# Performance work log

Measured on AMD Instinct MI355X. Metric: run time of the kernel, lower is better.

The kernel has to match this reference:

```python
import jax, jax.numpy as jnp
import numpy as np

N = 50000
E = 800000
G = 64  # number of graphs in each batch
IN_DIM = 128
HID = 64
NEG_SLOPE = 0.2


def _glorot(key, shape):
    fan = shape[0] + shape[-1] if len(shape) == 2 else int(np.prod(shape[1:])) + shape[-1]
    lim = float(np.sqrt(6.0 / fan))
    return jax.random.uniform(key, shape, jnp.float32, -lim, lim)


def setup_inputs() -> dict:
    key = jax.random.key(0)
    ks = jax.random.split(key, 16)
    x1 = jax.random.normal(ks[0], (N, IN_DIM), jnp.float32)
    x2 = jax.random.normal(ks[1], (N, IN_DIM), jnp.float32)
    edge_index1 = jax.random.randint(ks[2], (2, E), 0, N, jnp.int64)
    edge_index2 = jax.random.randint(ks[3], (2, E), 0, N, jnp.int64)
    batch1 = jnp.sort(jax.random.randint(ks[4], (N,), 0, G, jnp.int64))
    batch2 = jnp.sort(jax.random.randint(ks[5], (N,), 0, G, jnp.int64))
    # conv1: GATConv(IN_DIM, HID, heads=4)
    W1 = _glorot(ks[6], (IN_DIM, 4 * HID))
    a_src1 = _glorot(ks[7], (1, 4, HID))
    a_dst1 = _glorot(ks[8], (1, 4, HID))
    b1 = jnp.zeros((4 * HID,), jnp.float32)
    # conv2: GATConv(4*HID, HID, heads=1)
    W2 = _glorot(ks[9], (4 * HID, HID))
    a_src2 = _glorot(ks[10], (1, 1, HID))
    a_dst2 = _glorot(ks[11], (1, 1, HID))
    b2 = jnp.zeros((HID,), jnp.float32)
    return {"x1": x1, "edge_index1": edge_index1, "batch1": batch1,
            "x2": x2, "edge_index2": edge_index2, "batch2": batch2,
            "W1": W1, "a_src1": a_src1, "a_dst1": a_dst1, "b1": b1,
            "W2": W2, "a_src2": a_src2, "a_dst2": a_dst2, "b2": b2}


def gat_conv(x, src, dst, W, a_src, a_dst, b, n_nodes, heads, out_dim):
    """PyG GATConv with add_self_loops=True, negative_slope=0.2, concat=True."""
    h = (x @ W).reshape(n_nodes, heads, out_dim)            # [N,H,D]
    alpha_s = jnp.sum(h * a_src, axis=-1)                   # [N,H]
    alpha_d = jnp.sum(h * a_dst, axis=-1)                   # [N,H]
    e = alpha_s[src] + alpha_d[dst]                         # [E',H]
    e = jax.nn.leaky_relu(e, NEG_SLOPE)
    # segment softmax over incoming edges of each destination node
    e_max = jax.ops.segment_max(e, dst, num_segments=n_nodes)
    ex = jnp.exp(e - e_max[dst])
    denom = jax.ops.segment_sum(ex, dst, num_segments=n_nodes)
    alpha = ex / (denom[dst] + 1e-16)                       # [E',H]
    msg = h[src] * alpha[:, :, None]                        # [E',H,D]
    out = jax.ops.segment_sum(msg, dst, num_segments=n_nodes)
    return out.reshape(n_nodes, heads * out_dim) + b


def embed(x, edge_index, batch, W1, a_src1, a_dst1, b1, W2, a_src2, a_dst2, b2):
    loops = jnp.arange(N, dtype=edge_index.dtype)
    src = jnp.concatenate([edge_index[0], loops])
    dst = jnp.concatenate([edge_index[1], loops])
    h = jax.nn.elu(gat_conv(x, src, dst, W1, a_src1, a_dst1, b1, N, 4, HID))
    h = jax.nn.elu(gat_conv(h, src, dst, W2, a_src2, a_dst2, b2, N, 1, HID))
    # global_mean_pool over graph ids
    sums = jax.ops.segment_sum(h, batch, num_segments=G)
    cnt = jax.ops.segment_sum(jnp.ones((N,), h.dtype), batch, num_segments=G)
    return sums / jnp.maximum(cnt, 1.0)[:, None]


def reference(x1, edge_index1, batch1, x2, edge_index2, batch2,
              W1, a_src1, a_dst1, b1, W2, a_src2, a_dst2, b2):
    emb1 = embed(x1, edge_index1, batch1, W1, a_src1, a_dst1, b1, W2, a_src2, a_dst2, b2)
    emb2 = embed(x2, edge_index2, batch2, W1, a_src1, a_dst1, b1, W2, a_src2, a_dst2, b2)
    return (emb1, emb2)
```

## Files before the change

kernel.cpp:

```cpp
#include <hip/hip_runtime.h>
#include <cstdint>
#include <cstddef>

#define NNODES 50000
#define NEDGES 800000
#define NGR    64
#define INDIM  128
#define HIDD   64
#define DCAP   64
#define NBUCK  391
#define BCAP   2560

typedef __attribute__((ext_vector_type(8))) _Float16 f16x8;
typedef __attribute__((ext_vector_type(2))) _Float16 half2v;
typedef __attribute__((ext_vector_type(4))) float f32x4;
typedef __attribute__((ext_vector_type(2))) float f32x2;

__device__ __forceinline__ float lrelu(float x) { return x > 0.f ? x : 0.2f * x; }
__device__ __forceinline__ float eluf(float x)  { return x > 0.f ? x : expm1f(x); }
__device__ __forceinline__ unsigned short f2h(float x) {
    _Float16 h = (_Float16)x;
    return __builtin_bit_cast(unsigned short, h);
}
__device__ __forceinline__ float h2f(unsigned short u) {
    return (float)__builtin_bit_cast(_Float16, u);
}
__device__ __forceinline__ float h2lo(unsigned int u) {
    half2v h = __builtin_bit_cast(half2v, u);
    return (float)h.x;
}
__device__ __forceinline__ float h2hi(unsigned int u) {
    half2v h = __builtin_bit_cast(half2v, u);
    return (float)h.y;
}

__global__ void cvt_f2h(const float* __restrict__ in, unsigned short* __restrict__ out, int n4) {
    int i = blockIdx.x * 256 + threadIdx.x;
    if (i < n4) {
        float4 v = ((const float4*)in)[i];
        ushort4 o;
        o.x = f2h(v.x); o.y = f2h(v.y); o.z = f2h(v.z); o.w = f2h(v.w);
        ((ushort4*)out)[i] = o;
    }
}

__global__ void cvt_d16(const int* __restrict__ ei0, const int* __restrict__ ei1,
                        unsigned short* __restrict__ d16, int E) {
    int g = blockIdx.y;
    const int* dd = (g ? ei1 : ei0) + E;
    unsigned short* o = d16 + (size_t)g * E;
    int i = blockIdx.x * 256 + threadIdx.x;
    if (i < E / 4) {
        int4 v = ((const int4*)dd)[i];
        ushort4 t;
        t.x = (unsigned short)v.x; t.y = (unsigned short)v.y;
        t.z = (unsigned short)v.z; t.w = (unsigned short)v.w;
        ((ushort4*)o)[i] = t;
    }
}

__global__ __launch_bounds__(256) void proj_ws(const float* __restrict__ W1f,
                                               const float* __restrict__ a_src,
                                               const float* __restrict__ a_dst,
                                               float* __restrict__ proj) {
    int o = blockIdx.x * 256 + threadIdx.x;
    if (o >= 1024) return;
    int sd = o >> 9, h = (o >> 7) & 3, k = o & 127;
    const float* av = sd ? a_dst : a_src;
    float s = 0.f;
    #pragma unroll 8
    for (int d = 0; d < 64; d++)
        s += W1f[k * 256 + h * 64 + d] * av[h * 64 + d];
    proj[o] = s;
}

__global__ __launch_bounds__(256) void cvt_xa(const float* __restrict__ x0,
                                              const float* __restrict__ x1,
                                              const float* __restrict__ proj,
                                              unsigned short* __restrict__ x16,
                                              float* __restrict__ as1,
                                              float* __restrict__ ad1, int n) {
    int gph = blockIdx.y;
    const float* xf = (gph ? x1 : x0);
    unsigned short* xo = x16 + (size_t)gph * n * 128;
    float* aso = as1 + (size_t)gph * n * 4;
    float* ado = ad1 + (size_t)gph * n * 4;
    int wave = threadIdx.x >> 6, lane = threadIdx.x & 63;
    int node = blockIdx.x * 4 + wave;
    if (node >= n) return;
    float2 v = *(const float2*)(xf + (size_t)node * 128 + lane * 2);
    ushort2 t; t.x = f2h(v.x); t.y = f2h(v.y);
    *(unsigned int*)(xo + (size_t)node * 128 + lane * 2) =
        __builtin_bit_cast(unsigned int, t);
    float ps[4], pd[4];
    #pragma unroll
    for (int h = 0; h < 4; h++) {
        float2 ws = *(const float2*)(proj + h * 128 + lane * 2);
        float2 wd = *(const float2*)(proj + 512 + h * 128 + lane * 2);
        ps[h] = v.x * ws.x + v.y * ws.y;
        pd[h] = v.x * wd.x + v.y * wd.y;
    }
    #pragma unroll
    for (int off = 1; off < 64; off <<= 1) {
        #pragma unroll
        for (int h = 0; h < 4; h++) {
            ps[h] += __shfl_xor(ps[h], off, 64);
            pd[h] += __shfl_xor(pd[h], off, 64);
        }
    }
    if (lane == 0) {
        *(float4*)(aso + node * 4) = make_float4(ps[0], ps[1], ps[2], ps[3]);
        *(float4*)(ado + node * 4) = make_float4(pd[0], pd[1], pd[2], pd[3]);
    }
}

__global__ __launch_bounds__(256) void bucket_p1(const int* __restrict__ ei0,
                                                 const int* __restrict__ ei1,
                                                 const unsigned short* __restrict__ d16_,
                                                 int* __restrict__ bcnt,
                                                 unsigned int* __restrict__ breg,
                                                 int E) {
    int g = blockIdx.y;
    const int* srcv = g ? ei1 : ei0;
    const unsigned short* d16 = d16_ + (size_t)g * E;
    int* bc = bcnt + g * NBUCK;
    unsigned int* br = breg + (size_t)g * NBUCK * BCAP;
    __shared__ int hist[NBUCK];
    __shared__ int base[NBUCK];
    int tid = threadIdx.x;
    int e0 = blockIdx.x * 4096;
    for (int i = tid; i < NBUCK; i += 256) hist[i] = 0;
    __syncthreads();
    int d[16], s[16];
    #pragma unroll
    for (int k = 0; k < 16; k++) {
        int e = e0 + k * 256 + tid;
        d[k] = -1; s[k] = 0;
        if (e < E) {
            d[k] = d16[e];
            s[k] = srcv[e];
            atomicAdd(&hist[d[k] >> 7], 1);
        }
    }
    __syncthreads();
    for (int i = tid; i < NBUCK; i += 256) {
        int c = hist[i];
        base[i] = c ? atomicAdd(&bc[i], c) : 0;
    }
    __syncthreads();
    for (int i = tid; i < NBUCK; i += 256) hist[i] = 0;
    __syncthreads();
    #pragma unroll
    for (int k = 0; k < 16; k++) {
        if (d[k] >= 0) {
            int b = d[k] >> 7;
            int r = atomicAdd(&hist[b], 1);
            int gp = base[b] + r;
            if (gp < BCAP)
                br[(size_t)b * BCAP + gp] =
                    (unsigned int)s[k] | ((unsigned int)(d[k] & 127) << 16);
        }
    }
}

__global__ __launch_bounds__(256) void bucket_p2(const unsigned int* __restrict__ breg,
                                                 const int* __restrict__ bcnt,
                                                 int* __restrict__ fc,
                                                 int* __restrict__ clpad, int N) {
    int g = blockIdx.y, b = blockIdx.x;
    __shared__ int rows[128 * DCAP];
    __shared__ int cnt[128];
    int tid = threadIdx.x;
    for (int i = tid; i < 128; i += 256) cnt[i] = 0;
    __syncthreads();
    int nE = bcnt[g * NBUCK + b]; if (nE > BCAP) nE = BCAP;
    const unsigned int* reg = breg + ((size_t)g * NBUCK + b) * BCAP;
    for (int e = tid; e < nE; e += 256) {
        unsigned int v = reg[e];
        int ln = v >> 16;
        int pos = atomicAdd(&cnt[ln], 1);
        if (pos < DCAP) rows[ln * DCAP + pos] = (int)(v & 0xffffu);
    }
    __syncthreads();
    int nodeBase = b * 128;
    for (int i = tid; i < 128; i += 256) {
        int node = nodeBase + i;
        if (node < N) fc[g * N + node] = cnt[i];
    }
    for (int i = tid; i < 128 * (DCAP / 4); i += 256) {
        int node = nodeBase + (i >> 4);
        if (node < N)
            ((uint4*)clpad)[((size_t)g * N + node) * (DCAP / 4) + (i & 15)] =
                ((const uint4*)rows)[i];
    }
}

__global__ __launch_bounds__(256) void agg_x4(const unsigned short* __restrict__ x16,
                                              const float* __restrict__ as_,
                                              const float* __restrict__ ad_,
                                              const int* __restrict__ fc,
                                              const int* __restrict__ cl,
                                              unsigned short* __restrict__ z,
                                              int n, int gph) {
    const unsigned short* xg = x16 + (size_t)gph * n * 128;
    const float* as = as_ + (size_t)gph * n * 4;
    const float* adp = ad_ + (size_t)gph * n * 4;
    const int* fcg = fc + gph * n;
    const int* clp = cl + (size_t)gph * n * DCAP;

    int wave = threadIdx.x >> 6, lane = threadIdx.x & 63;
    int node = blockIdx.x * 4 + wave;
    if (node >= n) return;
    int p = lane >> 4;
    int c = lane & 15;
    int l15 = lane & 15, quad = lane >> 4;
    float adv_q = adp[node * 4 + quad];

    float w0[4];
    #pragma unroll
    for (int h = 0; h < 4; h++)
        w0[h] = __expf(lrelu(as[node * 4 + h] + adp[node * 4 + h]));
    uint4 hu = *(const uint4*)(xg + (size_t)node * 128 + c * 8);
    f32x2 xs0 = {h2lo(hu.x), h2hi(hu.x)}, xs1 = {h2lo(hu.y), h2hi(hu.y)};
    f32x2 xs2 = {h2lo(hu.z), h2hi(hu.z)}, xs3 = {h2lo(hu.w), h2hi(hu.w)};
    float den[4];
    f32x2 acc[4][4];
    #pragma unroll
    for (int h = 0; h < 4; h++) {
        float m0 = (p == 0) ? w0[h] : 0.f;
        den[h] = m0;
        f32x2 m2 = {m0, m0};
        acc[h][0] = xs0 * m2; acc[h][1] = xs1 * m2;
        acc[h][2] = xs2 * m2; acc[h][3] = xs3 * m2;
    }
    int deg = __builtin_amdgcn_readfirstlane(fcg[node]);
    if (deg > DCAP) deg = DCAP;
    int beg = node * DCAP;
    for (int j = 0; j < deg; j += 16) {
        int m = deg - j; if (m > 16) m = 16;
        int colv = clp[beg + j + (l15 < m ? l15 : m - 1)];
        float wl = __expf(lrelu(as[colv * 4 + quad] + adv_q));
        int ec0 = (p)      < m ? (p)      : m - 1;
        int ec1 = (4 + p)  < m ? (4 + p)  : m - 1;
        int ec2 = (8 + p)  < m ? (8 + p)  : m - 1;
        int ec3 = (12 + p) < m ? (12 + p) : m - 1;
        int s0 = __shfl(colv, ec0), s1 = __shfl(colv, ec1);
        int s2 = __shfl(colv, ec2), s3 = __shfl(colv, ec3);
        uint4 u0 = *(const uint4*)(xg + (size_t)s0 * 128 + c * 8);
        uint4 u1 = *(const uint4*)(xg + (size_t)s1 * 128 + c * 8);
        uint4 u2 = *(const uint4*)(xg + (size_t)s2 * 128 + c * 8);
        uint4 u3 = *(const uint4*)(xg + (size_t)s3 * 128 + c * 8);
        auto step = [&](uint4 u, int e, int ec) {
            f32x2 xv0 = {h2lo(u.x), h2hi(u.x)};
            f32x2 xv1 = {h2lo(u.y), h2hi(u.y)};
            f32x2 xv2 = {h2lo(u.z), h2hi(u.z)};
            f32x2 xv3 = {h2lo(u.w), h2hi(u.w)};
            #pragma unroll
            for (int h = 0; h < 4; h++) {
                float we = __shfl(wl, (h << 4) | ec);
                if (e >= m) we = 0.f;
                den[h] += we;
                f32x2 w2 = {we, we};
                acc[h][0] += xv0 * w2;
                acc[h][1] += xv1 * w2;
                acc[h][2] += xv2 * w2;
                acc[h][3] += xv3 * w2;
            }
        };
        step(u0, p, ec0);
        if (m > 4)  step(u1, 4 + p, ec1);
        if (m > 8)  step(u2, 8 + p, ec2);
        if (m > 12) step(u3, 12 + p, ec3);
    }
    #pragma unroll
    for (int off = 16; off < 64; off <<= 1) {
        #pragma unroll
        for (int h = 0; h < 4; h++) {
            den[h] += __shfl_xor(den[h], off);
            #pragma unroll
            for (int k = 0; k < 4; k++) {
                acc[h][k].x += __shfl_xor(acc[h][k].x, off);
                acc[h][k].y += __shfl_xor(acc[h][k].y, off);
            }
        }
    }
    if (p == 0) {
        #pragma unroll
        for (int h = 0; h < 4; h++) {
            float rden = 1.f / (den[h] + 1e-16f);
            unsigned short t[8];
            #pragma unroll
            for (int k = 0; k < 4; k++) {
                t[2 * k]     = f2h(acc[h][k].x * rden);
                t[2 * k + 1] = f2h(acc[h][k].y * rden);
            }
            *(uint4*)(z + ((size_t)h * n + node) * 128 + c * 8) = *(uint4*)t;
        }
    }
}

__global__ __launch_bounds__(256) void gemm_z(const unsigned short* __restrict__ z,
                                              const unsigned short* __restrict__ W1h,
                                              const float* __restrict__ bias,
                                              unsigned short* __restrict__ g1,
                                              int M, int gph) {
    constexpr int BM = 128, BK = 64, LDA = BK + 8;
    __shared__ unsigned short Asm[BM * LDA];
    __shared__ unsigned short Bsm[64 * LDA];
    int h = blockIdx.z;
    const unsigned short* Az = z + (size_t)h * M * 128;
    unsigned short* Cg = g1 + (size_t)gph * M * 256;
    int c0 = h * 64;
    int tid = threadIdx.x, lane = tid & 63, wave = tid >> 6;
    int l15 = lane & 15, quad = lane >> 4;
    int wm0 = wave * 32;
    int row0 = blockIdx.x * BM;

    f32x4 acc[2][4];
    #pragma unroll
    for (int mi = 0; mi < 2; mi++)
        #pragma unroll
        for (int ni = 0; ni < 4; ni++)
            acc[mi][ni] = (f32x4){0.f, 0.f, 0.f, 0.f};

    for (int k0 = 0; k0 < 128; k0 += BK) {
        #pragma unroll
        for (int q = 0; q < 4; q++) {
            int idx = q * 256 + tid;
            int r = idx >> 3, kc = idx & 7;
            int row = row0 + r;
            uint4 v = make_uint4(0u, 0u, 0u, 0u);
            if (row < M) v = *(const uint4*)(Az + (size_t)row * 128 + k0 + kc * 8);
            *(uint4*)&Asm[r * LDA + kc * 8] = v;
        }
        #pragma unroll
        for (int q = 0; q < 2; q++) {
            int idx = q * 256 + tid;
            int n = idx & 63;
            int kc = idx >> 6;
            unsigned short tmp[8];
            #pragma unroll
            for (int j = 0; j < 8; j++)
                tmp[j] = W1h[(size_t)(k0 + kc * 8 + j) * 256 + c0 + n];
            *(uint4*)&Bsm[n * LDA + kc * 8] = *(uint4*)tmp;
        }
        __syncthreads();
        #pragma unroll
        for (int kb = 0; kb < 2; kb++) {
            f16x8 af[2], bfr[4];
            #pragma unroll
            for (int mi = 0; mi < 2; mi++)
                af[mi] = *(f16x8*)&Asm[(wm0 + mi * 16 + l15) * LDA + kb * 32 + quad * 8];
            #pragma unroll
            for (int ni = 0; ni < 4; ni++)
                bfr[ni] = *(f16x8*)&Bsm[(ni * 16 + l15) * LDA + kb * 32 + quad * 8];
            #pragma unroll
            for (int mi = 0; mi < 2; mi++)
                #pragma unroll
                for (int ni = 0; ni < 4; ni++)
                    acc[mi][ni] = __builtin_amdgcn_mfma_f32_16x16x32_f16(
                        af[mi], bfr[ni], acc[mi][ni], 0, 0, 0);
        }
        __syncthreads();
    }
    #pragma unroll
    for (int mi = 0; mi < 2; mi++) {
        #pragma unroll
        for (int r = 0; r < 4; r++) {
            int row = row0 + wm0 + mi * 16 + quad * 4 + r;
            if (row < M) {
                #pragma unroll
                for (int ni = 0; ni < 4; ni++) {
                    int colg = c0 + ni * 16 + l15;
                    Cg[(size_t)row * 256 + colg] = f2h(eluf(acc[mi][ni][r] + bias[colg]));
                }
            }
        }
    }
}

template<int BN, int WM, int WN>
__global__ __launch_bounds__(256) void gemm_mfma(const unsigned short* __restrict__ A0,
                                                 size_t Ags,
                                                 const unsigned short* __restrict__ Bw,
                                                 unsigned short* __restrict__ C,
                                                 size_t Cgs,
                                                 int M, int K, int N,
                                                 const float* __restrict__ a_src,
                                                 const float* __restrict__ a_dst,
                                                 float* __restrict__ as_o,
                                                 float* __restrict__ ad_o,
                                                 int hstride, int ags) {
    constexpr int BM = 128, BK = 64;
    constexpr int MI = WM / 16, NI = WN / 16;
    constexpr int LDA = BK + 8;
    __shared__ unsigned short Asm[BM * LDA];
    __shared__ unsigned short Bsm[BN * LDA];
    int gph = blockIdx.z;
    const unsigned short* Ab = A0 + (size_t)gph * Ags;
    unsigned short* Cg = C + (size_t)gph * Cgs;
    float* aso = as_o + (size_t)gph * ags;
    float* ado = ad_o + (size_t)gph * ags;
    int tid = threadIdx.x;
    int lane = tid & 63, wave = tid >> 6;
    int l15 = lane & 15, quad = lane >> 4;
    int wm0 = wave * 32, wn0 = 0;
    int row0 = blockIdx.x * BM;
    int c0 = blockIdx.y * BN;

    f32x4 acc[MI][NI];
    #pragma unroll
    for (int mi = 0; mi < MI; mi++)
        #pragma unroll
        for (int ni = 0; ni < NI; ni++)
            acc[mi][ni] = (f32x4){0.f, 0.f, 0.f, 0.f};

    for (int k0 = 0; k0 < K; k0 += BK) {
        #pragma unroll
        for (int q = 0; q < BM / 32; q++) {
            int idx = q * 256 + tid;
            int r = idx >> 3, kc = idx & 7;
            int row = row0 + r;
            uint4 v = make_uint4(0u, 0u, 0u, 0u);
            if (row < M) v = *(const uint4*)(Ab + (size_t)row * K + k0 + kc * 8);
            *(uint4*)&Asm[r * LDA + kc * 8] = v;
        }
        #pragma unroll
        for (int q = 0; q < BN / 32; q++) {
            int idx = q * 256 + tid;
            int n  = idx & (BN - 1);
            int kc = idx / BN;
            unsigned short tmp[8];
            #pragma unroll
            for (int j = 0; j < 8; j++)
                tmp[j] = Bw[(size_t)(k0 + kc * 8 + j) * N + c0 + n];
            *(uint4*)&Bsm[n * LDA + kc * 8] = *(uint4*)tmp;
        }
        __syncthreads();
        #pragma unroll
        for (int kb = 0; kb < 2; kb++) {
            f16x8 af[MI], bfr[NI];
            #pragma unroll
            for (int mi = 0; mi < MI; mi++)
                af[mi] = *(f16x8*)&Asm[(wm0 + mi * 16 + l15) * LDA + kb * 32 + quad * 8];
            #pragma unroll
            for (int ni = 0; ni < NI; ni++)
                bfr[ni] = *(f16x8*)&Bsm[(wn0 + ni * 16 + l15) * LDA + kb * 32 + quad * 8];
            #pragma unroll
            for (int mi = 0; mi < MI; mi++)
                #pragma unroll
                for (int ni = 0; ni < NI; ni++)
                    acc[mi][ni] = __builtin_amdgcn_mfma_f32_16x16x32_f16(
                        af[mi], bfr[ni], acc[mi][ni], 0, 0, 0);
        }
        __syncthreads();
    }
    #pragma unroll
    for (int mi = 0; mi < MI; mi++) {
        #pragma unroll
        for (int r = 0; r < 4; r++) {
            int row = row0 + wm0 + mi * 16 + quad * 4 + r;
            if (row < M) {
                #pragma unroll
                for (int ni = 0; ni < NI; ni++) {
                    int colg = c0 + wn0 + ni * 16 + l15;
                    Cg[(size_t)row * N + colg] = f2h(acc[mi][ni][r]);
                }
            }
        }
    }
    int headc = (c0 + wn0) >> 6;
    float a_s[NI], a_d[NI];
    #pragma unroll
    for (int ni = 0; ni < NI; ni++) {
        a_s[ni] = a_src[headc * 64 + ni * 16 + l15];
        a_d[ni] = a_dst[headc * 64 + ni * 16 + l15];
    }
    #pragma unroll
    for (int mi = 0; mi < MI; mi++) {
        #pragma unroll
        for (int r = 0; r < 4; r++) {
            float ps = 0.f, pd = 0.f;
            #pragma unroll
            for (int ni = 0; ni < NI; ni++) {
                ps += acc[mi][ni][r] * a_s[ni];
                pd += acc[mi][ni][r] * a_d[ni];
            }
            #pragma unroll
            for (int off = 1; off < 16; off <<= 1) {
                ps += __shfl_xor(ps, off, 64);
                pd += __shfl_xor(pd, off, 64);
            }
            int row = row0 + wm0 + mi * 16 + quad * 4 + r;
            if (l15 == 0 && row < M) {
                aso[row * hstride + headc] = ps;
                ado[row * hstride + headc] = pd;
            }
        }
    }
}

__global__ __launch_bounds__(256) void agg_h1(const unsigned short* __restrict__ h,
                                              size_t hgs,
                                              const float* __restrict__ as_,
                                              const float* __restrict__ ad_,
                                              const int* __restrict__ fc,
                                              const int* __restrict__ cl,
                                              const float* __restrict__ bias,
                                              float* __restrict__ out,
                                              size_t ogs, int n) {
    int gph = blockIdx.y;
    const uint4* h4 = (const uint4*)(h + (size_t)gph * hgs);
    const float* as = as_ + (size_t)gph * n;
    const float* adp = ad_ + (size_t)gph * n;
    const int* fcg = fc + gph * n;
    const int* clp = cl + (size_t)gph * n * DCAP;
    float* og = out + (size_t)gph * ogs;

    int wave = threadIdx.x >> 6, lane = threadIdx.x & 63;
    int node = blockIdx.x * 4 + wave;
    if (node >= n) return;
    int p = lane >> 3;
    int c = lane & 7;
    float adv = adp[node];
    float w0 = __expf(lrelu(as[node] + adv));
    float m0 = (p == 0) ? w0 : 0.f;
    uint4 hu = h4[(size_t)node * 8 + c];
    float den = m0;
    float a0 = h2lo(hu.x) * m0, a1 = h2hi(hu.x) * m0;
    float a2 = h2lo(hu.y) * m0, a3 = h2hi(hu.y) * m0;
    float a4 = h2lo(hu.z) * m0, a5 = h2hi(hu.z) * m0;
    float a6 = h2lo(hu.w) * m0, a7 = h2hi(hu.w) * m0;
    int deg = __builtin_amdgcn_readfirstlane(fcg[node]);
    if (deg > DCAP) deg = DCAP;
    if (deg > 0) {
        int colv = clp[node * DCAP + (lane < deg ? lane : deg - 1)];
        float wl = __expf(lrelu(as[colv] + adv));
        for (int base = 0; base < deg; base += 8) {
            int e = base + p;
            int ec = e < deg ? e : deg - 1;
            float we = __shfl(wl, ec);
            if (e >= deg) we = 0.f;
            int s = __shfl(colv, ec);
            uint4 u = h4[(size_t)s * 8 + c];
            den += we;
            a0 = fmaf(h2lo(u.x), we, a0); a1 = fmaf(h2hi(u.x), we, a1);
            a2 = fmaf(h2lo(u.y), we, a2); a3 = fmaf(h2hi(u.y), we, a3);
            a4 = fmaf(h2lo(u.z), we, a4); a5 = fmaf(h2hi(u.z), we, a5);
            a6 = fmaf(h2lo(u.w), we, a6); a7 = fmaf(h2hi(u.w), we, a7);
        }
    }
    #pragma unroll
    for (int off = 8; off < 64; off <<= 1) {
        den += __shfl_xor(den, off);
        a0 += __shfl_xor(a0, off); a1 += __shfl_xor(a1, off);
        a2 += __shfl_xor(a2, off); a3 += __shfl_xor(a3, off);
        a4 += __shfl_xor(a4, off); a5 += __shfl_xor(a5, off);
        a6 += __shfl_xor(a6, off); a7 += __shfl_xor(a7, off);
    }
    if (p == 0) {
        float rden = 1.f / (den + 1e-16f);
        float4 b0 = ((const float4*)bias)[c * 2];
        float4 b1 = ((const float4*)bias)[c * 2 + 1];
        float4 o0, o1;
        o0.x = eluf(a0 * rden + b0.x); o0.y = eluf(a1 * rden + b0.y);
        o0.z = eluf(a2 * rden + b0.z); o0.w = eluf(a3 * rden + b0.w);
        o1.x = eluf(a4 * rden + b1.x); o1.y = eluf(a5 * rden + b1.y);
        o1.z = eluf(a6 * rden + b1.z); o1.w = eluf(a7 * rden + b1.w);
        float* orow = og + (size_t)node * 64 + c * 8;
        *(float4*)orow = o0;
        *(float4*)(orow + 4) = o1;
    }
}

__device__ __forceinline__ int lbound(const int* __restrict__ a, int n, int key) {
    int lo = 0, hi = n;
    while (lo < hi) {
        int mid = (lo + hi) >> 1;
        if (a[mid] < key) lo = mid + 1; else hi = mid;
    }
    return lo;
}

__global__ __launch_bounds__(256) void pool_mean(const float* __restrict__ g2,
                                                 size_t ggs,
                                                 const int* __restrict__ b0,
                                                 const int* __restrict__ b1,
                                                 float* __restrict__ out, int n) {
    __shared__ float red[4][64];
    __shared__ int bnds[2];
    int gph = blockIdx.y;
    const int* batch = gph ? b1 : b0;
    const float* gg = g2 + (size_t)gph * ggs;
    float* og = out + (size_t)gph * NGR * HIDD;
    int g = blockIdx.x;
    if (threadIdx.x < 2) bnds[threadIdx.x] = lbound(batch, n, g + (int)threadIdx.x);
    __syncthreads();
    int s = bnds[0], e = bnds[1];
    int lane = threadIdx.x & 63, wave = threadIdx.x >> 6;
    float acc = 0.f;
    for (int i = s + wave; i < e; i += 4)
        acc += gg[(size_t)i * 64 + lane];
    red[wave][lane] = acc;
    __syncthreads();
    if (wave == 0) {
        float sum = red[0][lane] + red[1][lane] + red[2][lane] + red[3][lane];
        og[g * 64 + lane] = sum / fmaxf((float)(e - s), 1.0f);
    }
}

extern "C" void kernel_launch(void* const* d_in, const int* in_sizes, int n_in,
                              void* d_out, int out_size, void* d_ws, size_t ws_size,
                              hipStream_t stream) {
    const int N = NNODES, E = NEDGES;

    const float* x1 = (const float*)d_in[0];
    const float* x2 = (const float*)d_in[3];
    const int* ei1v = (const int*)d_in[1];
    const int* ei2v = (const int*)d_in[4];
    const int* ba1  = (const int*)d_in[2];
    const int* ba2  = (const int*)d_in[5];
    const float* W1     = (const float*)d_in[6];
    const float* a_src1 = (const float*)d_in[7];
    const float* a_dst1 = (const float*)d_in[8];
    const float* b1     = (const float*)d_in[9];
    const float* W2     = (const float*)d_in[10];
    const float* a_src2 = (const float*)d_in[11];
    const float* a_dst2 = (const float*)d_in[12];
    const float* b2     = (const float*)d_in[13];

    char* ws = (char*)d_ws;
    size_t off = 0;
    auto carve = [&](size_t bytes) -> char* {
        char* p = ws + off;
        off = (off + bytes + 255) & ~(size_t)255;
        return p;
    };
    unsigned short* x16 = (unsigned short*)carve((size_t)2 * N * 128 * 2);
    char* Rz = carve((size_t)4 * N * 128 * 2);
    unsigned short* g1 = (unsigned short*)carve((size_t)2 * N * 256 * 2);
    int*   clpad = (int*)carve((size_t)2 * N * DCAP * 4);
    unsigned short* d16 = (unsigned short*)carve((size_t)2 * E * 2);
    int*   fc   = (int*)carve((size_t)2 * N * 4);
    int*   bcnt = (int*)carve((size_t)2 * NBUCK * 4);
    float* as1  = (float*)carve((size_t)2 * N * 4 * 4);
    float* ad1  = (float*)carve((size_t)2 * N * 4 * 4);
    float* as2  = (float*)carve((size_t)2 * N * 4);
    float* ad2  = (float*)carve((size_t)2 * N * 4);
    float* proj = (float*)carve(2 * 4 * 128 * 4);
    unsigned short* W1h = (unsigned short*)carve(INDIM * 256 * 2);
    unsigned short* W2h = (unsigned short*)carve(256 * HIDD * 2);

    unsigned int* breg = (unsigned int*)Rz;
    unsigned short* zbuf = (unsigned short*)Rz;
    float* g2 = (float*)Rz;
    unsigned short* h2 = x16;

    float* outF = (float*)d_out;

    const int nodeBlocks = (N + 3) / 4;

    cvt_f2h<<<(INDIM * 256 / 4 + 255) / 256, 256, 0, stream>>>(W1, W1h, INDIM * 256 / 4);
    cvt_f2h<<<(256 * HIDD / 4 + 255) / 256, 256, 0, stream>>>(W2, W2h, 256 * HIDD / 4);
    proj_ws<<<4, 256, 0, stream>>>(W1, a_src1, a_dst1, proj);
    cvt_xa<<<dim3(nodeBlocks, 2), 256, 0, stream>>>(x1, x2, proj, x16, as1, ad1, N);
    cvt_d16<<<dim3((E / 4 + 255) / 256, 2), 256, 0, stream>>>(ei1v, ei2v, d16, E);

    hipMemsetAsync(bcnt, 0, (size_t)2 * NBUCK * 4, stream);
    bucket_p1<<<dim3((E + 4095) / 4096, 2), 256, 0, stream>>>(ei1v, ei2v, d16,
                                                              bcnt, breg, E);
    bucket_p2<<<dim3(NBUCK, 2), 256, 0, stream>>>(breg, bcnt, fc, clpad, N);

    agg_x4<<<nodeBlocks, 256, 0, stream>>>(x16, as1, ad1, fc, clpad, zbuf, N, 0);
    gemm_z<<<dim3(391, 1, 4), 256, 0, stream>>>(zbuf, W1h, b1, g1, N, 0);
    agg_x4<<<nodeBlocks, 256, 0, stream>>>(x16, as1, ad1, fc, clpad, zbuf, N, 1);
    gemm_z<<<dim3(391, 1, 4), 256, 0, stream>>>(zbuf, W1h, b1, g1, N, 1);

    gemm_mfma<64, 32, 64><<<dim3(391, 1, 2), 256, 0, stream>>>(
        g1, (size_t)N * 256, W2h, h2, (size_t)N * 64, N, 256, HIDD,
        a_src2, a_dst2, as2, ad2, 1, N);
    agg_h1<<<dim3(nodeBlocks, 2), 256, 0, stream>>>(h2, (size_t)N * 64, as2, ad2,
                                                    fc, clpad, b2, g2, (size_t)N * 64, N);

    pool_mean<<<dim3(NGR, 2), 256, 0, stream>>>(g2, (size_t)N * 64, ba1, ba2, outF, N);
}
```

Baseline: 506.9 us.

## Map two nodes per wave in layer-1 aggregation, drop cross-lane reduction

The first-layer attention aggregation kernel now gives each half-wave one destination node, so 32 lanes each own 4 feature columns. The old layout split edges across four lane groups and reduced them with shuffles. Each lane now walks all neighbours itself in chunks of 8, issuing the eight row gathers up front before accumulating, which removes the final shuffle reduction and the idle lanes at store time. The trade-off is narrower 8-byte loads per lane, and the two half-waves may have different degrees, which can cause divergence inside a wave.

```diff
diff --git a/kernel.cpp b/kernel.cpp
--- a/kernel.cpp
+++ b/kernel.cpp
@@ -209,93 +209,66 @@
     const int* clp = cl + (size_t)gph * n * DCAP;
 
     int wave = threadIdx.x >> 6, lane = threadIdx.x & 63;
-    int node = blockIdx.x * 4 + wave;
+    int half = lane >> 5;
+    int c = lane & 31;
+    int hb = half * 32;
+    int node = blockIdx.x * 8 + wave * 2 + half;
     if (node >= n) return;
-    int p = lane >> 4;
-    int c = lane & 15;
-    int l15 = lane & 15, quad = lane >> 4;
-    float adv_q = adp[node * 4 + quad];
+    int wh = c >> 3;
+    int wk = c & 7;
+    float adv_l = adp[node * 4 + wh];
 
     float w0[4];
     #pragma unroll
     for (int h = 0; h < 4; h++)
         w0[h] = __expf(lrelu(as[node * 4 + h] + adp[node * 4 + h]));
-    uint4 hu = *(const uint4*)(xg + (size_t)node * 128 + c * 8);
-    f32x2 xs0 = {h2lo(hu.x), h2hi(hu.x)}, xs1 = {h2lo(hu.y), h2hi(hu.y)};
-    f32x2 xs2 = {h2lo(hu.z), h2hi(hu.z)}, xs3 = {h2lo(hu.w), h2hi(hu.w)};
+    uint2 hu = *(const uint2*)(xg + (size_t)node * 128 + c * 4);
+    f32x2 xv0 = {h2lo(hu.x), h2hi(hu.x)}, xv1 = {h2lo(hu.y), h2hi(hu.y)};
     float den[4];
-    f32x2 acc[4][4];
+    f32x2 acc[4][2];
     #pragma unroll
     for (int h = 0; h < 4; h++) {
-        float m0 = (p == 0) ? w0[h] : 0.f;
-        den[h] = m0;
-        f32x2 m2 = {m0, m0};
-        acc[h][0] = xs0 * m2; acc[h][1] = xs1 * m2;
-        acc[h][2] = xs2 * m2; acc[h][3] = xs3 * m2;
-    }
-    int deg = __builtin_amdgcn_readfirstlane(fcg[node]);
+        den[h] = w0[h];
+        f32x2 m2 = {w0[h], w0[h]};
+        acc[h][0] = xv0 * m2;
+        acc[h][1] = xv1 * m2;
+    }
+    int deg = fcg[node];
     if (deg > DCAP) deg = DCAP;
     int beg = node * DCAP;
-    for (int j = 0; j < deg; j += 16) {
-        int m = deg - j; if (m > 16) m = 16;
-        int colv = clp[beg + j + (l15 < m ? l15 : m - 1)];
-        float wl = __expf(lrelu(as[colv * 4 + quad] + adv_q));
-        int ec0 = (p)      < m ? (p)      : m - 1;
-        int ec1 = (4 + p)  < m ? (4 + p)  : m - 1;
-        int ec2 = (8 + p)  < m ? (8 + p)  : m - 1;
-        int ec3 = (12 + p) < m ? (12 + p) : m - 1;
-        int s0 = __shfl(colv, ec0), s1 = __shfl(colv, ec1);
-        int s2 = __shfl(colv, ec2), s3 = __shfl(colv, ec3);
-        uint4 u0 = *(const uint4*)(xg + (size_t)s0 * 128 + c * 8);
-        uint4 u1 = *(const uint4*)(xg + (size_t)s1 * 128 + c * 8);
-        uint4 u2 = *(const uint4*)(xg + (size_t)s2 * 128 + c * 8);
-        uint4 u3 = *(const uint4*)(xg + (size_t)s3 * 128 + c * 8);
-        auto step = [&](uint4 u, int e, int ec) {
-            f32x2 xv0 = {h2lo(u.x), h2hi(u.x)};
-            f32x2 xv1 = {h2lo(u.y), h2hi(u.y)};
-            f32x2 xv2 = {h2lo(u.z), h2hi(u.z)};
-            f32x2 xv3 = {h2lo(u.w), h2hi(u.w)};
-            #pragma unroll
-            for (int h = 0; h < 4; h++) {
-                float we = __shfl(wl, (h << 4) | ec);
-                if (e >= m) we = 0.f;
-                den[h] += we;
-                f32x2 w2 = {we, we};
-                acc[h][0] += xv0 * w2;
-                acc[h][1] += xv1 * w2;
-                acc[h][2] += xv2 * w2;
-                acc[h][3] += xv3 * w2;
+    for (int j = 0; j < deg; j += 8) {
+        int m = deg - j; if (m > 8) m = 8;
+        int colv = clp[beg + j + (wk < m ? wk : m - 1)];
+        float wl = __expf(lrelu(as[colv * 4 + wh] + adv_l));
+        uint2 u[8];
+        #pragma unroll
+        for (int k = 0; k < 8; k++) {
+            int sk = __shfl(colv, hb + (k < m ? k : m - 1));
+            u[k] = *(const uint2*)(xg + (size_t)sk * 128 + c * 4);
+        }
+        #pragma unroll
+        for (int k = 0; k < 8; k++) {
+            if (k < m) {
+                f32x2 a0 = {h2lo(u[k].x), h2hi(u[k].x)};
+                f32x2 a1 = {h2lo(u[k].y), h2hi(u[k].y)};
+                #pragma unroll
+                for (int h = 0; h < 4; h++) {
+                    float we = __shfl(wl, hb + h * 8 + k);
+                    den[h] += we;
+                    f32x2 w2 = {we, we};
+                    acc[h][0] += a0 * w2;
+                    acc[h][1] += a1 * w2;
+                }
             }
-        };
-        step(u0, p, ec0);
-        if (m > 4)  step(u1, 4 + p, ec1);
-        if (m > 8)  step(u2, 8 + p, ec2);
-        if (m > 12) step(u3, 12 + p, ec3);
-    }
-    #pragma unroll
-    for (int off = 16; off < 64; off <<= 1) {
-        #pragma unroll
-        for (int h = 0; h < 4; h++) {
-            den[h] += __shfl_xor(den[h], off);
-            #pragma unroll
-            for (int k = 0; k < 4; k++) {
-                acc[h][k].x += __shfl_xor(acc[h][k].x, off);
-                acc[h][k].y += __shfl_xor(acc[h][k].y, off);
-            }
-        }
-    }
-    if (p == 0) {
-        #pragma unroll
-        for (int h = 0; h < 4; h++) {
-            float rden = 1.f / (den[h] + 1e-16f);
-            unsigned short t[8];
-            #pragma unroll
-            for (int k = 0; k < 4; k++) {
-                t[2 * k]     = f2h(acc[h][k].x * rden);
-                t[2 * k + 1] = f2h(acc[h][k].y * rden);
-            }
-            *(uint4*)(z + ((size_t)h * n + node) * 128 + c * 8) = *(uint4*)t;
-        }
+        }
+    }
+    #pragma unroll
+    for (int h = 0; h < 4; h++) {
+        float rden = 1.f / (den[h] + 1e-16f);
+        ushort4 t;
+        t.x = f2h(acc[h][0].x * rden); t.y = f2h(acc[h][0].y * rden);
+        t.z = f2h(acc[h][1].x * rden); t.w = f2h(acc[h][1].y * rden);
+        *(uint2*)(z + ((size_t)h * n + node) * 128 + c * 4) = *(uint2*)&t;
     }
 }
 
@@ -671,9 +644,9 @@
                                                               bcnt, breg, E);
     bucket_p2<<<dim3(NBUCK, 2), 256, 0, stream>>>(breg, bcnt, fc, clpad, N);
 
-    agg_x4<<<nodeBlocks, 256, 0, stream>>>(x16, as1, ad1, fc, clpad, zbuf, N, 0);
+    agg_x4<<<(N + 7) / 8, 256, 0, stream>>>(x16, as1, ad1, fc, clpad, zbuf, N, 0);
     gemm_z<<<dim3(391, 1, 4), 256, 0, stream>>>(zbuf, W1h, b1, g1, N, 0);
-    agg_x4<<<nodeBlocks, 256, 0, stream>>>(x16, as1, ad1, fc, clpad, zbuf, N, 1);
+    agg_x4<<<(N + 7) / 8, 256, 0, stream>>>(x16, as1, ad1, fc, clpad, zbuf, N, 1);
     gemm_z<<<dim3(391, 1, 4), 256, 0, stream>>>(zbuf, W1h, b1, g1, N, 1);
 
     gemm_mfma<64, 32, 64><<<dim3(391, 1, 2), 256, 0, stream>>>(
```

Result: faster. 473.7 us (-6.6%).
